# Performance work log

Hardware: AMD Instinct MI355X
Metric: run time of the kernel (lower is better)

Reference implementation:

```python
import jax, jax.numpy as jnp
import numpy as np

B, S, D = 2, 2048, 1024
H = 16
HD = D // H  # 64


def setup_inputs() -> dict:
    key = jax.random.key(0)
    ks = jax.random.split(key, 6)
    scale = 1.0 / np.sqrt(D)
    return {
        "x": jax.random.normal(ks[0], (B, S, D), dtype=jnp.float32),
        "W_q": jax.random.normal(ks[1], (D, D), dtype=jnp.float32) * scale,
        "W_k": jax.random.normal(ks[2], (D, D), dtype=jnp.float32) * scale,
        "W_v": jax.random.normal(ks[3], (D, D), dtype=jnp.float32) * scale,
        "W_o": jax.random.normal(ks[4], (D, D), dtype=jnp.float32) * scale,
        "b_o": jax.random.normal(ks[5], (D,), dtype=jnp.float32) * 0.01,
    }


def reference(x, W_q, W_k, W_v, W_o, b_o):
    # Projections (torch Linear applies x @ W.T; weights here stored as [out, in])
    q = jnp.einsum("bsd,ed->bse", x, W_q).reshape(B, S, H, HD)
    k = jnp.einsum("bsd,ed->bse", x, W_k).reshape(B, S, H, HD)
    v = jnp.einsum("bsd,ed->bse", x, W_v).reshape(B, S, H, HD)
    # scores: [B, H, S, S]
    scores = jnp.einsum("bqhd,bkhd->bhqk", q, k) / jnp.sqrt(jnp.float32(HD))
    attn = jax.nn.softmax(scores, axis=-1)
    # dropout is identity in eval mode
    out = jnp.einsum("bhqk,bkhd->bqhd", attn, v).reshape(B, S, D)
    return jnp.einsum("bsd,ed->bse", out, W_o) + b_o
```

## Files before the change

kernel.cpp:

```cpp
#include <hip/hip_runtime.h>
#include <hip/hip_bf16.h>

typedef __hip_bfloat16 bf16_t;
typedef __bf16 bf16x8 __attribute__((ext_vector_type(8)));
typedef __bf16 bf16x4 __attribute__((ext_vector_type(4)));
typedef short  s16x4  __attribute__((ext_vector_type(4)));
typedef float  f32x4  __attribute__((ext_vector_type(4)));

#define MFMA(a, b, c) __builtin_amdgcn_mfma_f32_16x16x32_bf16((a), (b), (c), 0, 0, 0)

__device__ __forceinline__ f32x4 mfma16(bf16x4 a, bf16x4 b, f32x4 c) {
#if __has_builtin(__builtin_amdgcn_mfma_f32_16x16x16_bf16)
  return __builtin_amdgcn_mfma_f32_16x16x16_bf16(a, b, c, 0, 0, 0);
#else
  return __builtin_amdgcn_mfma_f32_16x16x16bf16_1k(
      __builtin_bit_cast(s16x4, a), __builtin_bit_cast(s16x4, b), c, 0, 0, 0);
#endif
}

__device__ __forceinline__ float fast_exp2(float x) {
#if __has_builtin(__builtin_amdgcn_exp2f)
  return __builtin_amdgcn_exp2f(x);
#else
  float r;
  asm("v_exp_f32 %0, %1" : "=v"(r) : "v"(x));
  return r;
#endif
}

__device__ __forceinline__ bf16x8 ldg8(const bf16_t* p) {
  return *reinterpret_cast<const bf16x8*>(p);
}
__device__ __forceinline__ bf16x4 ldg4(const bf16_t* p) {
  return *reinterpret_cast<const bf16x4*>(p);
}
__device__ __forceinline__ void st8(bf16_t* p, bf16x8 v) {
  *reinterpret_cast<bf16x8*>(p) = v;
}
__device__ __forceinline__ void store_out(bf16_t* p, float v) { *p = __float2bfloat16(v); }
__device__ __forceinline__ void store_out(float* p, float v)  { *p = v; }

__device__ __forceinline__ void async16(const bf16_t* g, bf16_t* l) {
  __builtin_amdgcn_global_load_lds(
      (const __attribute__((address_space(1))) void*)g,
      (__attribute__((address_space(3))) void*)l, 16, 0, 0);
}

__global__ __launch_bounds__(256) void cvt_kernel(
    const float* __restrict__ x,  const float* __restrict__ Wq,
    const float* __restrict__ Wk, const float* __restrict__ Wv,
    const float* __restrict__ Wo,
    bf16_t* __restrict__ xb,  bf16_t* __restrict__ Wqb,
    bf16_t* __restrict__ Wkb, bf16_t* __restrict__ Wvb,
    bf16_t* __restrict__ Wob) {
  const int bid = blockIdx.x;
  const float* src; bf16_t* dst; size_t base;
  float scl = 1.0f;
  if (bid < 2048)      { src = x;  dst = xb;  base = (size_t)bid * 2048; }
  else if (bid < 2560) { src = Wq; dst = Wqb; base = (size_t)(bid - 2048) * 2048;
                         scl = 0.180336878f; }
  else if (bid < 3072) { src = Wk; dst = Wkb; base = (size_t)(bid - 2560) * 2048; }
  else if (bid < 3584) { src = Wv; dst = Wvb; base = (size_t)(bid - 3072) * 2048; }
  else                 { src = Wo; dst = Wob; base = (size_t)(bid - 3584) * 2048; }
  const size_t i0 = base + (size_t)threadIdx.x * 8;
  const float4 f0 = *reinterpret_cast<const float4*>(src + i0);
  const float4 f1 = *reinterpret_cast<const float4*>(src + i0 + 4);
  bf16x8 v;
  v[0] = (__bf16)(f0.x * scl); v[1] = (__bf16)(f0.y * scl);
  v[2] = (__bf16)(f0.z * scl); v[3] = (__bf16)(f0.w * scl);
  v[4] = (__bf16)(f1.x * scl); v[5] = (__bf16)(f1.y * scl);
  v[6] = (__bf16)(f1.z * scl); v[7] = (__bf16)(f1.w * scl);
  st8(dst + i0, v);
}

#define GK 1024

template <typename OutT, bool BIAS>
__device__ __forceinline__ void gemm_tile(
    const bf16_t* __restrict__ A, const bf16_t* __restrict__ B,
    OutT* __restrict__ C, const float* __restrict__ bias,
    int bm, int bn, int ldc, bf16_t* As, bf16_t* Bs) {
  const int tid  = threadIdx.x;
  const int lane = tid & 63;
  const int wave = tid >> 6;
  const int wm   = (wave & 1) << 6;
  const int wn   = (wave >> 1) << 6;
  const int lr   = lane & 15;
  const int lq   = lane >> 4;

  const int srow = tid >> 3;
  const int sx   = ((tid & 7) ^ (srow & 7)) << 3;

  const bf16_t* Ag = A + (size_t)(bm + srow) * GK + sx;
  const bf16_t* Bg = B + (size_t)(bn + srow) * GK + sx;
  bf16_t* Asw = As + wave * 512;
  bf16_t* Bsw = Bs + wave * 512;

  f32x4 acc[4][4];
#pragma unroll
  for (int i = 0; i < 4; ++i)
#pragma unroll
    for (int j = 0; j < 4; ++j) acc[i][j] = (f32x4){0.f, 0.f, 0.f, 0.f};

  for (int k0 = 0; k0 < GK; k0 += 64) {
    __syncthreads();
#pragma unroll
    for (int g = 0; g < 4; ++g) {
      async16(Ag + k0 + (size_t)(g * 32) * GK, Asw + g * 2048);
      async16(Bg + k0 + (size_t)(g * 32) * GK, Bsw + g * 2048);
    }
    __syncthreads();
#pragma unroll
    for (int ks = 0; ks < 2; ++ks) {
      bf16x8 af[4], bf[4];
      const int chs = ((ks * 4 + lq) ^ (lr & 7)) << 3;
#pragma unroll
      for (int i = 0; i < 4; ++i) {
        af[i] = ldg8(&As[(wm + i * 16 + lr) * 64 + chs]);
        bf[i] = ldg8(&Bs[(wn + i * 16 + lr) * 64 + chs]);
      }
#pragma unroll
      for (int mi = 0; mi < 4; ++mi)
#pragma unroll
        for (int ni = 0; ni < 4; ++ni)
          acc[mi][ni] = MFMA(af[mi], bf[ni], acc[mi][ni]);
    }
  }

#pragma unroll
  for (int ni = 0; ni < 4; ++ni) {
    const int col = bn + wn + ni * 16 + lr;
    float bv = 0.f;
    if (BIAS) bv = bias[col];
#pragma unroll
    for (int mi = 0; mi < 4; ++mi) {
#pragma unroll
      for (int r = 0; r < 4; ++r) {
        const int row = bm + wm + mi * 16 + lq * 4 + r;
        store_out(&C[(size_t)row * ldc + col], acc[mi][ni][r] + bv);
      }
    }
  }
}

__global__ __launch_bounds__(256) void qkv_kernel(
    const bf16_t* __restrict__ x, const bf16_t* __restrict__ Wq,
    const bf16_t* __restrict__ Wk, const bf16_t* __restrict__ Wv,
    bf16_t* __restrict__ Q, bf16_t* __restrict__ Kp, bf16_t* __restrict__ Vt) {
  __shared__ alignas(16) bf16_t As[128 * 64];
  __shared__ alignas(16) bf16_t Bs[128 * 64];
  const int bid = blockIdx.x;
  const int z   = blockIdx.y;
  const int mt  = (bid & 31) * 128;
  const int nt  = (bid >> 5) * 128;
  if (z == 0) {
    gemm_tile<bf16_t, false>(x, Wq, Q, nullptr, mt, nt, 1024, As, Bs);
  } else if (z == 1) {
    gemm_tile<bf16_t, false>(x, Wk, Kp, nullptr, mt, nt, 1024, As, Bs);
  } else {
    gemm_tile<bf16_t, false>(Wv, x, Vt, nullptr, nt, mt, 4096, As, Bs);
  }
}

__global__ __launch_bounds__(256) void out_proj_kernel(
    const bf16_t* __restrict__ Ao, const bf16_t* __restrict__ Wo,
    const float* __restrict__ bias, float* __restrict__ out) {
  __shared__ alignas(16) bf16_t As[128 * 64];
  __shared__ alignas(16) bf16_t Bs[128 * 64];
  const int bid = blockIdx.x;
  gemm_tile<float, true>(Ao, Wo, out, bias, (bid & 31) * 128, (bid >> 5) * 128, 1024, As, Bs);
}

#define VPAD 68

__global__ __launch_bounds__(256, 2) void attn_kernel(
    const bf16_t* __restrict__ Q, const bf16_t* __restrict__ Kp,
    const bf16_t* __restrict__ Vt, bf16_t* __restrict__ Ao) {
  __shared__ alignas(16) char smem_raw[2 * 8192 + 2 * 8704];
  bf16_t* Ks0 = (bf16_t*)smem_raw;
  bf16_t* Ks1 = Ks0 + 4096;
  bf16_t* Vs0 = (bf16_t*)(smem_raw + 16384);
  bf16_t* Vs1 = Vs0 + 64 * VPAD;
  float*  Osc = (float*)smem_raw;

  const int tid  = threadIdx.x;
  const int lane = tid & 63;
  const int wave = tid >> 6;
  const int lr   = lane & 15;
  const int lq   = lane >> 4;
  const int bh   = blockIdx.x;
  const int qt   = blockIdx.y;
  const int b    = bh >> 4;
  const int h    = bh & 15;
  const size_t tok0 = (size_t)b * 2048;
  const int col0 = h * 64;
  const int qblk = qt * 128 + wave * 32;

  bf16x8 qf[2][2];
#pragma unroll
  for (int nt = 0; nt < 2; ++nt) {
    const size_t qrow = tok0 + qblk + nt * 16 + lr;
#pragma unroll
    for (int c = 0; c < 2; ++c)
      qf[nt][c] = ldg8(&Q[qrow * 1024 + col0 + c * 32 + lq * 8]);
  }

  f32x4 o[2][4];
#pragma unroll
  for (int nt = 0; nt < 2; ++nt)
#pragma unroll
    for (int i = 0; i < 4; ++i) o[nt][i] = (f32x4){0.f, 0.f, 0.f, 0.f};
  float lsum[2] = {0.f, 0.f};

  const int srow = tid >> 3;
  const int sxk  = ((tid & 7) ^ (srow & 7)) << 3;
  const int sxv  = (tid & 7) << 3;
  const int kdst = wave * 512;

  const int koff0 = lr * 64 + ((lq ^ (lr & 7)) << 3);
  const int koff1 = lr * 64 + (((lq + 4) ^ (lr & 7)) << 3);
  const int voff  = lr * VPAD + lq * 4;

  const bf16_t* Kg0 = Kp + tok0 * 1024 + col0;
  const bf16_t* Vg0 = Vt + (size_t)col0 * 4096 + tok0;

  auto stage_k = [&](const bf16_t* Kg, bf16_t* Ksn) {
    async16(Kg + (size_t)srow * 1024 + sxk, Ksn + kdst);
    async16(Kg + (size_t)(srow + 32) * 1024 + sxk, Ksn + kdst + 2048);
  };

  auto compute_tile = [&](const bf16_t* Ksc, const bf16_t* Vsc) {
#pragma unroll
    for (int c = 0; c < 4; ++c) {
      const bf16x8 kf0 = ldg8(&Ksc[c * 1024 + koff0]);
      const bf16x8 kf1 = ldg8(&Ksc[c * 1024 + koff1]);
      bf16x4 pb[2];
#pragma unroll
      for (int nt = 0; nt < 2; ++nt) {
        f32x4 sT = {0.f, 0.f, 0.f, 0.f};
        sT = MFMA(kf0, qf[nt][0], sT);
        sT = MFMA(kf1, qf[nt][1], sT);
        const float p0 = fast_exp2(sT.x);
        const float p1 = fast_exp2(sT.y);
        const float p2 = fast_exp2(sT.z);
        const float p3 = fast_exp2(sT.w);
        pb[nt][0] = (__bf16)p0; pb[nt][1] = (__bf16)p1;
        pb[nt][2] = (__bf16)p2; pb[nt][3] = (__bf16)p3;
        lsum[nt] += (p0 + p1) + (p2 + p3);
      }
#pragma unroll
      for (int ht = 0; ht < 4; ++ht) {
        const bf16x4 vf = ldg4(&Vsc[ht * 16 * VPAD + voff + c * 16]);
        o[0][ht] = mfma16(vf, pb[0], o[0][ht]);
        o[1][ht] = mfma16(vf, pb[1], o[1][ht]);
      }
    }
  };

  {
    const bf16x8 v0 = ldg8(Vg0 + (size_t)srow * 4096 + sxv);
    const bf16x8 v1 = ldg8(Vg0 + (size_t)(srow + 32) * 4096 + sxv);
    stage_k(Kg0, Ks0);
    st8(&Vs0[srow * VPAD + sxv], v0);
    st8(&Vs0[(srow + 32) * VPAD + sxv], v1);
  }

#pragma unroll 1
  for (int t = 0; t < 32; t += 2) {
    __syncthreads();
    {
      const bf16_t* Kg = Kg0 + (size_t)(t + 1) * 65536;
      const bf16_t* Vg = Vg0 + (t + 1) * 64;
      const bf16x8 v0 = ldg8(Vg + (size_t)srow * 4096 + sxv);
      const bf16x8 v1 = ldg8(Vg + (size_t)(srow + 32) * 4096 + sxv);
      stage_k(Kg, Ks1);
      compute_tile(Ks0, Vs0);
      st8(&Vs1[srow * VPAD + sxv], v0);
      st8(&Vs1[(srow + 32) * VPAD + sxv], v1);
    }
    __syncthreads();
    if (t + 2 < 32) {
      const bf16_t* Kg = Kg0 + (size_t)(t + 2) * 65536;
      const bf16_t* Vg = Vg0 + (t + 2) * 64;
      const bf16x8 v0 = ldg8(Vg + (size_t)srow * 4096 + sxv);
      const bf16x8 v1 = ldg8(Vg + (size_t)(srow + 32) * 4096 + sxv);
      stage_k(Kg, Ks0);
      compute_tile(Ks1, Vs1);
      st8(&Vs0[srow * VPAD + sxv], v0);
      st8(&Vs0[(srow + 32) * VPAD + sxv], v1);
    } else {
      compute_tile(Ks1, Vs1);
    }
  }

  __syncthreads();

  float* Ow = &Osc[wave * 64 * 17];
#pragma unroll
  for (int nt = 0; nt < 2; ++nt) {
    float ls = lsum[nt];
    ls += __shfl_xor(ls, 16);
    ls += __shfl_xor(ls, 32);
    const float invl = 1.f / ls;

#pragma unroll
    for (int ht = 0; ht < 4; ++ht)
#pragma unroll
      for (int r = 0; r < 4; ++r)
        Ow[(ht * 16 + lq * 4 + r) * 17 + lr] = o[nt][ht][r] * invl;

    const int qq = lane >> 2;
    const int hc = (lane & 3) * 16;
    bf16x8 w0, w1;
#pragma unroll
    for (int i = 0; i < 8; ++i) {
      w0[i] = (__bf16)Ow[(hc + i) * 17 + qq];
      w1[i] = (__bf16)Ow[(hc + 8 + i) * 17 + qq];
    }
    bf16_t* dst = Ao + (tok0 + qblk + nt * 16 + qq) * 1024 + col0 + hc;
    st8(dst, w0);
    st8(dst + 8, w1);
  }
}

extern "C" void kernel_launch(void* const* d_in, const int* in_sizes, int n_in,
                              void* d_out, int out_size, void* d_ws, size_t ws_size,
                              hipStream_t stream) {
  const float* x  = (const float*)d_in[0];
  const float* Wq = (const float*)d_in[1];
  const float* Wk = (const float*)d_in[2];
  const float* Wv = (const float*)d_in[3];
  const float* Wo = (const float*)d_in[4];
  const float* bo = (const float*)d_in[5];
  float* out = (float*)d_out;

  const size_t NTOK = 4096, DMODEL = 1024, WSZ = DMODEL * DMODEL;
  bf16_t* xb  = (bf16_t*)d_ws;
  bf16_t* Wqb = xb + NTOK * DMODEL;
  bf16_t* Wkb = Wqb + WSZ;
  bf16_t* Wvb = Wkb + WSZ;
  bf16_t* Wob = Wvb + WSZ;
  bf16_t* Q   = Wob + WSZ;
  bf16_t* Kp  = Q  + NTOK * DMODEL;
  bf16_t* Vt  = Kp + NTOK * DMODEL;
  bf16_t* Ao  = Vt + NTOK * DMODEL;

  cvt_kernel<<<dim3(4096), 256, 0, stream>>>(x, Wq, Wk, Wv, Wo, xb, Wqb, Wkb, Wvb, Wob);
  qkv_kernel<<<dim3(256, 3), 256, 0, stream>>>(xb, Wqb, Wkb, Wvb, Q, Kp, Vt);
  attn_kernel<<<dim3(32, 16), 256, 0, stream>>>(Q, Kp, Vt, Ao);
  out_proj_kernel<<<dim3(256, 1), 256, 0, stream>>>(Ao, Wob, bo, out);
}
```

Measured before the change: 184.2 us.

## Use 16x16x32 MFMA for PV by permuting K rows to match P layout

Replaces the 16x16x16 bf16 MFMA used for the P·V product with the wider 16x16x32 instruction, halving the number of PV MFMA issues and V LDS loads. To make the P fragments from two QK^T tiles line up with the 8-element K dimension of the larger MFMA, the K tile's LDS row mapping and XOR swizzle are reworked so each lane's score rows correspond to contiguous key positions. This depends on the new swizzle being consistent between the async stores and the fragment reads, and it changes bank-conflict behavior.

```diff
diff --git a/kernel.cpp b/kernel.cpp
--- a/kernel.cpp
+++ b/kernel.cpp
@@ -8,15 +8,6 @@
 typedef float  f32x4  __attribute__((ext_vector_type(4)));
 
 #define MFMA(a, b, c) __builtin_amdgcn_mfma_f32_16x16x32_bf16((a), (b), (c), 0, 0, 0)
-
-__device__ __forceinline__ f32x4 mfma16(bf16x4 a, bf16x4 b, f32x4 c) {
-#if __has_builtin(__builtin_amdgcn_mfma_f32_16x16x16_bf16)
-  return __builtin_amdgcn_mfma_f32_16x16x16_bf16(a, b, c, 0, 0, 0);
-#else
-  return __builtin_amdgcn_mfma_f32_16x16x16bf16_1k(
-      __builtin_bit_cast(s16x4, a), __builtin_bit_cast(s16x4, b), c, 0, 0, 0);
-#endif
-}
 
 __device__ __forceinline__ float fast_exp2(float x) {
 #if __has_builtin(__builtin_amdgcn_exp2f)
@@ -30,9 +21,6 @@
 
 __device__ __forceinline__ bf16x8 ldg8(const bf16_t* p) {
   return *reinterpret_cast<const bf16x8*>(p);
-}
-__device__ __forceinline__ bf16x4 ldg4(const bf16_t* p) {
-  return *reinterpret_cast<const bf16x4*>(p);
 }
 __device__ __forceinline__ void st8(bf16_t* p, bf16x8 v) {
   *reinterpret_cast<bf16x8*>(p) = v;
@@ -213,13 +201,20 @@
   float lsum[2] = {0.f, 0.f};
 
   const int srow = tid >> 3;
-  const int sxk  = ((tid & 7) ^ (srow & 7)) << 3;
+  const int fsw  = (srow & 3) | ((((srow >> 2) ^ (srow >> 3)) & 1) << 2);
+  const int sxk  = ((tid & 7) ^ fsw) << 3;
   const int sxv  = (tid & 7) << 3;
   const int kdst = wave * 512;
 
-  const int koff0 = lr * 64 + ((lq ^ (lr & 7)) << 3);
-  const int koff1 = lr * 64 + (((lq + 4) ^ (lr & 7)) << 3);
-  const int voff  = lr * VPAD + lq * 4;
+  const int fb  = (lr & 3) | (((lr >> 2) & 1) << 2);
+  const int x0  = (lq ^ fb) << 3;
+  const int rb  = ((lr >> 2) << 3) + (lr & 3);
+  const int k00 = rb * 64 + x0;
+  const int k01 = k00 ^ 32;
+  const int k10 = (rb + 4) * 64 + (x0 ^ 32);
+  const int k11 = k10 ^ 32;
+
+  const int voff8 = lr * VPAD + lq * 8;
 
   const bf16_t* Kg0 = Kp + tok0 * 1024 + col0;
   const bf16_t* Vg0 = Vt + (size_t)col0 * 4096 + tok0;
@@ -231,28 +226,34 @@
 
   auto compute_tile = [&](const bf16_t* Ksc, const bf16_t* Vsc) {
 #pragma unroll
-    for (int c = 0; c < 4; ++c) {
-      const bf16x8 kf0 = ldg8(&Ksc[c * 1024 + koff0]);
-      const bf16x8 kf1 = ldg8(&Ksc[c * 1024 + koff1]);
-      bf16x4 pb[2];
-#pragma unroll
-      for (int nt = 0; nt < 2; ++nt) {
-        f32x4 sT = {0.f, 0.f, 0.f, 0.f};
-        sT = MFMA(kf0, qf[nt][0], sT);
-        sT = MFMA(kf1, qf[nt][1], sT);
-        const float p0 = fast_exp2(sT.x);
-        const float p1 = fast_exp2(sT.y);
-        const float p2 = fast_exp2(sT.z);
-        const float p3 = fast_exp2(sT.w);
-        pb[nt][0] = (__bf16)p0; pb[nt][1] = (__bf16)p1;
-        pb[nt][2] = (__bf16)p2; pb[nt][3] = (__bf16)p3;
-        lsum[nt] += (p0 + p1) + (p2 + p3);
+    for (int c2 = 0; c2 < 2; ++c2) {
+      const bf16_t* Kh = Ksc + c2 * 2048;
+      bf16x8 pb[2];
+#pragma unroll
+      for (int cc = 0; cc < 2; ++cc) {
+        const bf16x8 kf0 = ldg8(&Kh[cc ? k10 : k00]);
+        const bf16x8 kf1 = ldg8(&Kh[cc ? k11 : k01]);
+#pragma unroll
+        for (int nt = 0; nt < 2; ++nt) {
+          f32x4 sT = {0.f, 0.f, 0.f, 0.f};
+          sT = MFMA(kf0, qf[nt][0], sT);
+          sT = MFMA(kf1, qf[nt][1], sT);
+          const float p0 = fast_exp2(sT.x);
+          const float p1 = fast_exp2(sT.y);
+          const float p2 = fast_exp2(sT.z);
+          const float p3 = fast_exp2(sT.w);
+          pb[nt][cc * 4 + 0] = (__bf16)p0;
+          pb[nt][cc * 4 + 1] = (__bf16)p1;
+          pb[nt][cc * 4 + 2] = (__bf16)p2;
+          pb[nt][cc * 4 + 3] = (__bf16)p3;
+          lsum[nt] += (p0 + p1) + (p2 + p3);
+        }
       }
 #pragma unroll
       for (int ht = 0; ht < 4; ++ht) {
-        const bf16x4 vf = ldg4(&Vsc[ht * 16 * VPAD + voff + c * 16]);
-        o[0][ht] = mfma16(vf, pb[0], o[0][ht]);
-        o[1][ht] = mfma16(vf, pb[1], o[1][ht]);
+        const bf16x8 vf = ldg8(&Vsc[ht * 16 * VPAD + voff8 + c2 * 32]);
+        o[0][ht] = MFMA(vf, pb[0], o[0][ht]);
+        o[1][ht] = MFMA(vf, pb[1], o[1][ht]);
       }
     }
   };
```

Measured after the change: 211.7 us. +14.9%, slower.

## Double-buffer GEMM shared-memory tiles with half-depth K stages

Applied to the files above, without the earlier changes.

The GEMM tile loop is restructured so each K=64 step is split into two K=32 stages held in two shared-memory buffers. The async copy of the next stage is issued before computing on the current one, so global loads overlap the MFMA work. Shared memory use stays the same, but the swizzle changes to suit 32-wide rows, and each stage does less MFMA work per barrier.

```diff
diff --git a/kernel.cpp b/kernel.cpp
--- a/kernel.cpp
+++ b/kernel.cpp
@@ -88,13 +88,16 @@
   const int lr   = lane & 15;
   const int lq   = lane >> 4;
 
-  const int srow = tid >> 3;
-  const int sx   = ((tid & 7) ^ (srow & 7)) << 3;
-
-  const bf16_t* Ag = A + (size_t)(bm + srow) * GK + sx;
-  const bf16_t* Bg = B + (size_t)(bn + srow) * GK + sx;
-  bf16_t* Asw = As + wave * 512;
-  bf16_t* Bsw = Bs + wave * 512;
+  const int srow4 = tid >> 2;
+  const int sxc   = ((tid & 3) ^ ((srow4 >> 1) & 3)) << 3;
+
+  const bf16_t* Ag = A + (size_t)(bm + srow4) * GK + sxc;
+  const bf16_t* Bg = B + (size_t)(bn + srow4) * GK + sxc;
+  const int kdst = wave * 512;
+
+  const int rchs  = (lq ^ ((lr >> 1) & 3)) << 3;
+  const int koffA = (wm + lr) * 32 + rchs;
+  const int koffB = (wn + lr) * 32 + rchs;
 
   f32x4 acc[4][4];
 #pragma unroll
@@ -102,29 +105,39 @@
 #pragma unroll
     for (int j = 0; j < 4; ++j) acc[i][j] = (f32x4){0.f, 0.f, 0.f, 0.f};
 
+  auto stage = [&](int k, bf16_t* Ap, bf16_t* Bp) {
+    async16(Ag + k, Ap + kdst);
+    async16(Ag + k + (size_t)64 * GK, Ap + kdst + 2048);
+    async16(Bg + k, Bp + kdst);
+    async16(Bg + k + (size_t)64 * GK, Bp + kdst + 2048);
+  };
+
+  auto compute = [&](const bf16_t* Ap, const bf16_t* Bp) {
+    bf16x8 af[4], bf[4];
+#pragma unroll
+    for (int i = 0; i < 4; ++i) {
+      af[i] = ldg8(&Ap[koffA + i * 512]);
+      bf[i] = ldg8(&Bp[koffB + i * 512]);
+    }
+#pragma unroll
+    for (int mi = 0; mi < 4; ++mi)
+#pragma unroll
+      for (int ni = 0; ni < 4; ++ni)
+        acc[mi][ni] = MFMA(af[mi], bf[ni], acc[mi][ni]);
+  };
+
+  bf16_t* As0 = As;          bf16_t* Bs0 = Bs;
+  bf16_t* As1 = As + 4096;   bf16_t* Bs1 = Bs + 4096;
+
+  stage(0, As0, Bs0);
+#pragma unroll 1
   for (int k0 = 0; k0 < GK; k0 += 64) {
     __syncthreads();
-#pragma unroll
-    for (int g = 0; g < 4; ++g) {
-      async16(Ag + k0 + (size_t)(g * 32) * GK, Asw + g * 2048);
-      async16(Bg + k0 + (size_t)(g * 32) * GK, Bsw + g * 2048);
-    }
+    stage(k0 + 32, As1, Bs1);
+    compute(As0, Bs0);
     __syncthreads();
-#pragma unroll
-    for (int ks = 0; ks < 2; ++ks) {
-      bf16x8 af[4], bf[4];
-      const int chs = ((ks * 4 + lq) ^ (lr & 7)) << 3;
-#pragma unroll
-      for (int i = 0; i < 4; ++i) {
-        af[i] = ldg8(&As[(wm + i * 16 + lr) * 64 + chs]);
-        bf[i] = ldg8(&Bs[(wn + i * 16 + lr) * 64 + chs]);
-      }
-#pragma unroll
-      for (int mi = 0; mi < 4; ++mi)
-#pragma unroll
-        for (int ni = 0; ni < 4; ++ni)
-          acc[mi][ni] = MFMA(af[mi], bf[ni], acc[mi][ni]);
-    }
+    if (k0 + 64 < GK) stage(k0 + 64, As0, Bs0);
+    compute(As1, Bs1);
   }
 
 #pragma unroll
@@ -147,8 +160,8 @@
     const bf16_t* __restrict__ x, const bf16_t* __restrict__ Wq,
     const bf16_t* __restrict__ Wk, const bf16_t* __restrict__ Wv,
     bf16_t* __restrict__ Q, bf16_t* __restrict__ Kp, bf16_t* __restrict__ Vt) {
-  __shared__ alignas(16) bf16_t As[128 * 64];
-  __shared__ alignas(16) bf16_t Bs[128 * 64];
+  __shared__ alignas(16) bf16_t As[2 * 128 * 32];
+  __shared__ alignas(16) bf16_t Bs[2 * 128 * 32];
   const int bid = blockIdx.x;
   const int z   = blockIdx.y;
   const int mt  = (bid & 31) * 128;
@@ -165,8 +178,8 @@
 __global__ __launch_bounds__(256) void out_proj_kernel(
     const bf16_t* __restrict__ Ao, const bf16_t* __restrict__ Wo,
     const float* __restrict__ bias, float* __restrict__ out) {
-  __shared__ alignas(16) bf16_t As[128 * 64];
-  __shared__ alignas(16) bf16_t Bs[128 * 64];
+  __shared__ alignas(16) bf16_t As[2 * 128 * 32];
+  __shared__ alignas(16) bf16_t Bs[2 * 128 * 32];
   const int bid = blockIdx.x;
   gemm_tile<float, true>(Ao, Wo, out, bias, (bid & 31) * 128, (bid >> 5) * 128, 1024, As, Bs);
 }
```

Result: slower. 188.9 us (+2.5%).

## Split attention work across eight waves with one query tile each

Applied to the files above, without the earlier changes.

The attention kernel now launches 512 threads per block instead of 256. Each wave handles 16 query rows instead of 32, and every thread stages a single K/V row chunk. This halves per-thread accumulator and Q-fragment registers and raises the requested occupancy, aiming to hide latency better. In exchange, each K/V fragment read from LDS feeds only one query tile, so LDS read traffic per MFMA doubles, and the tighter launch bound may constrain register allocation.

```diff
diff --git a/kernel.cpp b/kernel.cpp
--- a/kernel.cpp
+++ b/kernel.cpp
@@ -173,10 +173,10 @@
 
 #define VPAD 68
 
-__global__ __launch_bounds__(256, 2) void attn_kernel(
+__global__ __launch_bounds__(512, 4) void attn_kernel(
     const bf16_t* __restrict__ Q, const bf16_t* __restrict__ Kp,
     const bf16_t* __restrict__ Vt, bf16_t* __restrict__ Ao) {
-  __shared__ alignas(16) char smem_raw[2 * 8192 + 2 * 8704];
+  __shared__ alignas(16) char smem_raw[34816];
   bf16_t* Ks0 = (bf16_t*)smem_raw;
   bf16_t* Ks1 = Ks0 + 4096;
   bf16_t* Vs0 = (bf16_t*)(smem_raw + 16384);
@@ -194,23 +194,20 @@
   const int h    = bh & 15;
   const size_t tok0 = (size_t)b * 2048;
   const int col0 = h * 64;
-  const int qblk = qt * 128 + wave * 32;
-
-  bf16x8 qf[2][2];
-#pragma unroll
-  for (int nt = 0; nt < 2; ++nt) {
-    const size_t qrow = tok0 + qblk + nt * 16 + lr;
+  const int qblk = qt * 128 + wave * 16;
+
+  bf16x8 qf[2];
+  {
+    const size_t qrow = tok0 + qblk + lr;
 #pragma unroll
     for (int c = 0; c < 2; ++c)
-      qf[nt][c] = ldg8(&Q[qrow * 1024 + col0 + c * 32 + lq * 8]);
-  }
-
-  f32x4 o[2][4];
-#pragma unroll
-  for (int nt = 0; nt < 2; ++nt)
-#pragma unroll
-    for (int i = 0; i < 4; ++i) o[nt][i] = (f32x4){0.f, 0.f, 0.f, 0.f};
-  float lsum[2] = {0.f, 0.f};
+      qf[c] = ldg8(&Q[qrow * 1024 + col0 + c * 32 + lq * 8]);
+  }
+
+  f32x4 o[4];
+#pragma unroll
+  for (int i = 0; i < 4; ++i) o[i] = (f32x4){0.f, 0.f, 0.f, 0.f};
+  float lsum = 0.f;
 
   const int srow = tid >> 3;
   const int sxk  = ((tid & 7) ^ (srow & 7)) << 3;
@@ -226,7 +223,6 @@
 
   auto stage_k = [&](const bf16_t* Kg, bf16_t* Ksn) {
     async16(Kg + (size_t)srow * 1024 + sxk, Ksn + kdst);
-    async16(Kg + (size_t)(srow + 32) * 1024 + sxk, Ksn + kdst + 2048);
   };
 
   auto compute_tile = [&](const bf16_t* Ksc, const bf16_t* Vsc) {
@@ -234,35 +230,29 @@
     for (int c = 0; c < 4; ++c) {
       const bf16x8 kf0 = ldg8(&Ksc[c * 1024 + koff0]);
       const bf16x8 kf1 = ldg8(&Ksc[c * 1024 + koff1]);
-      bf16x4 pb[2];
-#pragma unroll
-      for (int nt = 0; nt < 2; ++nt) {
-        f32x4 sT = {0.f, 0.f, 0.f, 0.f};
-        sT = MFMA(kf0, qf[nt][0], sT);
-        sT = MFMA(kf1, qf[nt][1], sT);
-        const float p0 = fast_exp2(sT.x);
-        const float p1 = fast_exp2(sT.y);
-        const float p2 = fast_exp2(sT.z);
-        const float p3 = fast_exp2(sT.w);
-        pb[nt][0] = (__bf16)p0; pb[nt][1] = (__bf16)p1;
-        pb[nt][2] = (__bf16)p2; pb[nt][3] = (__bf16)p3;
-        lsum[nt] += (p0 + p1) + (p2 + p3);
-      }
+      f32x4 sT = {0.f, 0.f, 0.f, 0.f};
+      sT = MFMA(kf0, qf[0], sT);
+      sT = MFMA(kf1, qf[1], sT);
+      const float p0 = fast_exp2(sT.x);
+      const float p1 = fast_exp2(sT.y);
+      const float p2 = fast_exp2(sT.z);
+      const float p3 = fast_exp2(sT.w);
+      bf16x4 pb;
+      pb[0] = (__bf16)p0; pb[1] = (__bf16)p1;
+      pb[2] = (__bf16)p2; pb[3] = (__bf16)p3;
+      lsum += (p0 + p1) + (p2 + p3);
 #pragma unroll
       for (int ht = 0; ht < 4; ++ht) {
         const bf16x4 vf = ldg4(&Vsc[ht * 16 * VPAD + voff + c * 16]);
-        o[0][ht] = mfma16(vf, pb[0], o[0][ht]);
-        o[1][ht] = mfma16(vf, pb[1], o[1][ht]);
+        o[ht] = mfma16(vf, pb, o[ht]);
       }
     }
   };
 
   {
     const bf16x8 v0 = ldg8(Vg0 + (size_t)srow * 4096 + sxv);
-    const bf16x8 v1 = ldg8(Vg0 + (size_t)(srow + 32) * 4096 + sxv);
     stage_k(Kg0, Ks0);
     st8(&Vs0[srow * VPAD + sxv], v0);
-    st8(&Vs0[(srow + 32) * VPAD + sxv], v1);
   }
 
 #pragma unroll 1
@@ -272,22 +262,18 @@
       const bf16_t* Kg = Kg0 + (size_t)(t + 1) * 65536;
       const bf16_t* Vg = Vg0 + (t + 1) * 64;
       const bf16x8 v0 = ldg8(Vg + (size_t)srow * 4096 + sxv);
-      const bf16x8 v1 = ldg8(Vg + (size_t)(srow + 32) * 4096 + sxv);
       stage_k(Kg, Ks1);
       compute_tile(Ks0, Vs0);
       st8(&Vs1[srow * VPAD + sxv], v0);
-      st8(&Vs1[(srow + 32) * VPAD + sxv], v1);
     }
     __syncthreads();
     if (t + 2 < 32) {
       const bf16_t* Kg = Kg0 + (size_t)(t + 2) * 65536;
       const bf16_t* Vg = Vg0 + (t + 2) * 64;
       const bf16x8 v0 = ldg8(Vg + (size_t)srow * 4096 + sxv);
-      const bf16x8 v1 = ldg8(Vg + (size_t)(srow + 32) * 4096 + sxv);
       stage_k(Kg, Ks0);
       compute_tile(Ks1, Vs1);
       st8(&Vs0[srow * VPAD + sxv], v0);
-      st8(&Vs0[(srow + 32) * VPAD + sxv], v1);
     } else {
       compute_tile(Ks1, Vs1);
     }
@@ -296,9 +282,8 @@
   __syncthreads();
 
   float* Ow = &Osc[wave * 64 * 17];
-#pragma unroll
-  for (int nt = 0; nt < 2; ++nt) {
-    float ls = lsum[nt];
+  {
+    float ls = lsum;
     ls += __shfl_xor(ls, 16);
     ls += __shfl_xor(ls, 32);
     const float invl = 1.f / ls;
@@ -307,7 +292,7 @@
     for (int ht = 0; ht < 4; ++ht)
 #pragma unroll
       for (int r = 0; r < 4; ++r)
-        Ow[(ht * 16 + lq * 4 + r) * 17 + lr] = o[nt][ht][r] * invl;
+        Ow[(ht * 16 + lq * 4 + r) * 17 + lr] = o[ht][r] * invl;
 
     const int qq = lane >> 2;
     const int hc = (lane & 3) * 16;
@@ -317,7 +302,7 @@
       w0[i] = (__bf16)Ow[(hc + i) * 17 + qq];
       w1[i] = (__bf16)Ow[(hc + 8 + i) * 17 + qq];
     }
-    bf16_t* dst = Ao + (tok0 + qblk + nt * 16 + qq) * 1024 + col0 + hc;
+    bf16_t* dst = Ao + (tok0 + qblk + qq) * 1024 + col0 + hc;
     st8(dst, w0);
     st8(dst + 8, w1);
   }
@@ -347,6 +332,6 @@
 
   cvt_kernel<<<dim3(4096), 256, 0, stream>>>(x, Wq, Wk, Wv, Wo, xb, Wqb, Wkb, Wvb, Wob);
   qkv_kernel<<<dim3(256, 3), 256, 0, stream>>>(xb, Wqb, Wkb, Wvb, Q, Kp, Vt);
-  attn_kernel<<<dim3(32, 16), 256, 0, stream>>>(Q, Kp, Vt, Ao);
+  attn_kernel<<<dim3(32, 16), 512, 0, stream>>>(Q, Kp, Vt, Ao);
   out_proj_kernel<<<dim3(256, 1), 256, 0, stream>>>(Ao, Wob, bo, out);
 }
```

Measured after the change: 184.4 us. About the same (+0.1%).
